# Performance work log

Hardware: AMD Instinct MI355X
Metric: run time of the kernel (lower is better)

## Reference

```python
import jax, jax.numpy as jnp
import numpy as np
from jax import lax

C = 512
B, H, W = 16, 32, 32
PROP_ROUNDS = 5


def _conv(x, w, b, pad):
    # x: [B,Cin,H,W], w: [Cout,Cin,kh,kw]
    y = lax.conv_general_dilated(x, w, (1, 1), [(pad, pad), (pad, pad)],
                                 dimension_numbers=('NCHW', 'OIHW', 'NCHW'))
    return y + b[None, :, None, None]


def _attention(ex, q):
    # torch: A = ex_flat^T @ q_flat ; Bm = softmax(A^T, dim=1) ; att = q_flat @ Bm
    b, c, h, w = q.shape
    ef = ex.reshape(b, c, h * w)   # [B,C,N] exemplar positions n
    qf = q.reshape(b, c, h * w)    # [B,C,M] query positions m
    A = jnp.einsum('bcn,bcm->bnm', ef, qf)   # [B,N,M]
    S = jax.nn.softmax(A, axis=-1)           # softmax over query positions m
    att = jnp.einsum('bcm,bnm->bcn', qf, S)  # [B,C,N]
    return att.reshape(b, c, h, w)


def _gru(x, h, w_r, b_r, w_u, b_u, w_c, b_c):
    # standard ConvGRUCell, kernel_size=1 (padding 0)
    xh = jnp.concatenate([x, h], axis=1)
    r = jax.nn.sigmoid(_conv(xh, w_r, b_r, 0))
    u = jax.nn.sigmoid(_conv(xh, w_u, b_u, 0))
    c = jnp.tanh(_conv(jnp.concatenate([x, r * h], axis=1), w_c, b_c, 0))
    return h * (1.0 - u) + c * u


def setup_inputs() -> dict:
    key = jax.random.key(0)
    ks = jax.random.split(key, 8)
    f = lambda k, s: jax.random.normal(k, s, dtype=jnp.float32)
    return {
        'input1': f(ks[0], (B, C, H, W)),
        'input2': f(ks[1], (B, C, H, W)),
        'input3': f(ks[2], (B, C, H, W)),
        'w_fusion': f(ks[3], (C, 2 * C, 3, 3)) * 0.01,
        'b_fusion': jnp.zeros((C,), jnp.float32),
        'w_out': f(ks[4], (C, 2 * C, 3, 3)) * 0.01,
        'b_out': jnp.zeros((C,), jnp.float32),
        'w_reset': f(ks[5], (C, 2 * C, 1, 1)) * 0.01,
        'b_reset': jnp.zeros((C,), jnp.float32),
        'w_update': f(ks[6], (C, 2 * C, 1, 1)) * 0.01,
        'b_update': jnp.zeros((C,), jnp.float32),
        'w_cand': f(ks[7], (C, 2 * C, 1, 1)) * 0.01,
        'b_cand': jnp.zeros((C,), jnp.float32),
    }


def reference(input1, input2, input3, w_fusion, b_fusion, w_out, b_out,
              w_reset, b_reset, w_update, b_update, w_cand, b_cand):
    # Batched over B (per-item torch loop is mathematically independent per item).
    ex, q, q1 = input1, input2, input3
    gru = lambda x, h: _gru(x, h, w_reset, b_reset, w_update, b_update, w_cand, b_cand)
    for _ in range(PROP_ROUNDS):
        a1 = _conv(jnp.concatenate([_attention(ex, q), _attention(ex, q1)], 1), w_fusion, b_fusion, 1)
        a2 = _conv(jnp.concatenate([_attention(q, ex), _attention(q, q1)], 1), w_fusion, b_fusion, 1)
        a3 = _conv(jnp.concatenate([_attention(q1, ex), _attention(q1, q)], 1), w_fusion, b_fusion, 1)
        ex, q, q1 = gru(a1, ex), gru(a2, q), gru(a3, q1)
    x1 = _conv(jnp.concatenate([ex, input1], 1), w_out, b_out, 1)
    x2 = _conv(jnp.concatenate([q, input2], 1), w_out, b_out, 1)
    x3 = _conv(jnp.concatenate([q1, input3], 1), w_out, b_out, 1)
    return (x1, x2, x3)
```

## Files before the change

kernel.cpp:

```cpp
#include <hip/hip_runtime.h>
#include <hip/hip_bf16.h>


using bf16 = __hip_bfloat16;
typedef __attribute__((ext_vector_type(8))) short bf16x8;
typedef __attribute__((ext_vector_type(4))) float floatx4;

#define MFMA_BF16(a, b, c) __builtin_amdgcn_mfma_f32_16x16x32_bf16((a), (b), (c), 0, 0, 0)

__device__ __forceinline__ void gload_lds16(const bf16* g, bf16* l) {
  __builtin_amdgcn_global_load_lds(
      (__attribute__((address_space(1))) void*)(g),
      (__attribute__((address_space(3))) void*)(l), 16, 0, 0);
}

__device__ __forceinline__ int swz_off(int row, int seg) {
  return row * 32 + ((seg ^ ((row >> 1) & 3)) << 3);
}

__device__ __forceinline__ void stage128x32_async(const bf16* src, int ld,
                                                  bf16* lds, int tid) {
  int r = tid >> 2;
  int seg_log = (((tid & 3) ^ ((tid >> 3) & 3))) * 8;
  gload_lds16(src + (size_t)r * ld + seg_log, lds + tid * 8);
  gload_lds16(src + (size_t)(r + 64) * ld + seg_log, lds + tid * 8 + 2048);
}

__device__ __forceinline__ void mfma_tile(const bf16* la, const bf16* lb,
                                          int wm, int wn, int fm, int fq,
                                          floatx4 (&acc)[4][4]) {
  bf16x8 af[4], bfr[4];
#pragma unroll
  for (int i = 0; i < 4; i++)
    af[i] = *(const bf16x8*)(la + swz_off(wm + i * 16 + fm, fq));
#pragma unroll
  for (int j = 0; j < 4; j++)
    bfr[j] = *(const bf16x8*)(lb + swz_off(wn + j * 16 + fm, fq));
#pragma unroll
  for (int i = 0; i < 4; i++)
#pragma unroll
    for (int j = 0; j < 4; j++)
      acc[i][j] = MFMA_BF16(af[i], bfr[j], acc[i][j]);
}

__device__ __forceinline__ float sigmoidf_(float x) { return 1.0f / (1.0f + __expf(-x)); }
__device__ __forceinline__ unsigned short bfbits(float x) {
  bf16 h = __float2bfloat16(x);
  return *reinterpret_cast<unsigned short*>(&h);
}

__global__ void k_detect(const unsigned short* __restrict__ in, int* __restrict__ flag) {
  if (threadIdx.x == 0 && blockIdx.x == 0) {
    int cnt = 0;
    for (int i = 0; i < 512; i++) {
      int e = (in[i] >> 7) & 0xFF;
      if (e >= 114 && e <= 140) cnt++;
      }
    *flag = (cnt >= 450) ? 1 : 0;
  }
}

__global__ __launch_bounds__(256) void k_cvt(const void* __restrict__ src,
                                             bf16* __restrict__ dst,
                                             const int* __restrict__ flag, int n) {
  int i = blockIdx.x * 256 + threadIdx.x;
  if (i >= n) return;
  if (*flag)
    dst[i] = ((const bf16*)src)[i];
  else
    dst[i] = __float2bfloat16(((const float*)src)[i]);
}

__global__ __launch_bounds__(256, 2) void k_gram(const bf16* __restrict__ X,
                                                 const bf16* __restrict__ Y,
                                                 float* __restrict__ G) {
  int b = blockIdx.z;
  const bf16* Ab = X + (size_t)b * 524288 + (size_t)blockIdx.x * 128 * 512;
  const bf16* Bb = Y + (size_t)b * 524288 + (size_t)blockIdx.y * 128 * 512;
  __shared__ __align__(16) bf16 la[4096], lb[4096];
  int tid = threadIdx.x, wave = tid >> 6, lane = tid & 63;
  int wm = (wave & 1) * 64, wn = (wave >> 1) * 64, fm = lane & 15, fq = lane >> 4;
  floatx4 acc[4][4] = {};
  for (int kc = 0; kc < 512; kc += 32) {
    __syncthreads();
    stage128x32_async(Ab + kc, 512, la, tid);
    stage128x32_async(Bb + kc, 512, lb, tid);
    __syncthreads();
    mfma_tile(la, lb, wm, wn, fm, fq, acc);
  }
  size_t gb = (size_t)b * 1048576;
  int row0 = blockIdx.x * 128 + wm + fq * 4;
  int col0 = blockIdx.y * 128 + wn + fm;
#pragma unroll
  for (int i = 0; i < 4; i++)
#pragma unroll
    for (int j = 0; j < 4; j++)
#pragma unroll
      for (int r = 0; r < 4; r++)
        G[gb + (size_t)(row0 + i * 16 + r) * 1024 + col0 + j * 16] = acc[i][j][r];
}

__global__ __launch_bounds__(256) void k_softmax(float* __restrict__ G) {
  size_t row = blockIdx.x;
  float* g = G + row * 1024;
  int tid = threadIdx.x, wave = tid >> 6, lane = tid & 63;
  float4 x = ((const float4*)g)[tid];
  float m = fmaxf(fmaxf(x.x, x.y), fmaxf(x.z, x.w));
  for (int off = 32; off > 0; off >>= 1) m = fmaxf(m, __shfl_xor(m, off));
  __shared__ float red[4], red2[4];
  if (lane == 0) red[wave] = m;
  __syncthreads();
  m = fmaxf(fmaxf(red[0], red[1]), fmaxf(red[2], red[3]));
  float e0 = __expf(x.x - m), e1 = __expf(x.y - m);
  float e2 = __expf(x.z - m), e3 = __expf(x.w - m);
  float s = e0 + e1 + e2 + e3;
  for (int off = 32; off > 0; off >>= 1) s += __shfl_xor(s, off);
  if (lane == 0) red2[wave] = s;
  __syncthreads();
  float inv = 1.0f / (red2[0] + red2[1] + red2[2] + red2[3]);
  ushort4 o;
  o.x = bfbits(e0 * inv); o.y = bfbits(e1 * inv);
  o.z = bfbits(e2 * inv); o.w = bfbits(e3 * inv);
  ((ushort4*)((bf16*)g))[tid] = o;
}

__global__ __launch_bounds__(256, 2) void k_att(const bf16* __restrict__ S,
                                                const bf16* __restrict__ Ycn,
                                                bf16* __restrict__ out) {
  int b = blockIdx.z;
  const bf16* Ab = S + (size_t)b * 2097152 + (size_t)blockIdx.x * 128 * 2048;
  const bf16* Bb = Ycn + (size_t)b * 524288 + (size_t)blockIdx.y * 128 * 1024;
  __shared__ __align__(16) bf16 la[4096], lb[4096];
  int tid = threadIdx.x, wave = tid >> 6, lane = tid & 63;
  int wm = (wave & 1) * 64, wn = (wave >> 1) * 64, fm = lane & 15, fq = lane >> 4;
  floatx4 acc[4][4] = {};
  for (int kc = 0; kc < 1024; kc += 32) {
    __syncthreads();
    stage128x32_async(Ab + kc, 2048, la, tid);
    stage128x32_async(Bb + kc, 1024, lb, tid);
    __syncthreads();
    mfma_tile(la, lb, wm, wn, fm, fq, acc);
  }
  size_t ob = (size_t)b * 524288;
  int row0 = blockIdx.x * 128 + wm + fq * 4;
  int col0 = blockIdx.y * 128 + wn + fm;
#pragma unroll
  for (int i = 0; i < 4; i++)
#pragma unroll
    for (int j = 0; j < 4; j++)
#pragma unroll
      for (int r = 0; r < 4; r++)
        out[ob + (size_t)(row0 + i * 16 + r) * 512 + col0 + j * 16] =
            __float2bfloat16(acc[i][j][r]);
}

__global__ __launch_bounds__(256, 2) void k_gru01(const bf16* __restrict__ xb,
                                                  const bf16* __restrict__ hb,
                                                  const bf16* __restrict__ wR,
                                                  const bf16* __restrict__ bR,
                                                  const bf16* __restrict__ wU,
                                                  const bf16* __restrict__ bU,
                                                  bf16* __restrict__ rh_out,
                                                  bf16* __restrict__ u_out) {
  size_t row0 = (size_t)blockIdx.x * 128;
  int y = blockIdx.y;
  bool isR = (y < 4);
  int yy = isR ? y : (y - 4);
  const bf16* W = (isR ? wR : wU) + (size_t)yy * 128 * 1024;
  const bf16* bias = isR ? bR : bU;
  bf16* outp = isR ? rh_out : u_out;
  __shared__ __align__(16) bf16 la[4096], lb[4096];
  int tid = threadIdx.x, wave = tid >> 6, lane = tid & 63;
  int wm = (wave & 1) * 64, wn = (wave >> 1) * 64, fm = lane & 15, fq = lane >> 4;
  floatx4 acc[4][4] = {};
  for (int kc = 0; kc < 1024; kc += 32) {
    __syncthreads();
    const bf16* s_ = (kc < 512) ? (xb + row0 * 512 + kc) : (hb + row0 * 512 + (kc - 512));
    stage128x32_async(s_, 512, la, tid);
    stage128x32_async(W + kc, 1024, lb, tid);
    __syncthreads();
    mfma_tile(la, lb, wm, wn, fm, fq, acc);
  }
  int r0 = wm + fq * 4;
  int c0 = yy * 128 + wn + fm;
#pragma unroll
  for (int i = 0; i < 4; i++)
#pragma unroll
    for (int j = 0; j < 4; j++) {
      int co = c0 + j * 16;
      float bj = __bfloat162float(bias[co]);
#pragma unroll
      for (int r = 0; r < 4; r++) {
        size_t idx = (row0 + r0 + i * 16 + r) * 512 + co;
        float v = sigmoidf_(acc[i][j][r] + bj);
        if (isR)
          outp[idx] = __float2bfloat16(v * __bfloat162float(hb[idx]));
        else
          outp[idx] = __float2bfloat16(v);
      }
    }
}

__global__ __launch_bounds__(256, 2) void k_gru2(const bf16* __restrict__ xb,
                                                 const bf16* __restrict__ rhb,
                                                 const bf16* __restrict__ W,
                                                 const bf16* __restrict__ bias,
                                                 bf16* __restrict__ h_state,
                                                 const bf16* __restrict__ u_buf) {
  size_t row0 = (size_t)blockIdx.x * 128;
  const bf16* Wb = W + (size_t)blockIdx.y * 128 * 1024;
  __shared__ __align__(16) bf16 la[4096], lb[4096];
  int tid = threadIdx.x, wave = tid >> 6, lane = tid & 63;
  int wm = (wave & 1) * 64, wn = (wave >> 1) * 64, fm = lane & 15, fq = lane >> 4;
  floatx4 acc[4][4] = {};
  for (int kc = 0; kc < 1024; kc += 32) {
    __syncthreads();
    const bf16* s_ = (kc < 512) ? (xb + row0 * 512 + kc) : (rhb + row0 * 512 + (kc - 512));
    stage128x32_async(s_, 512, la, tid);
    stage128x32_async(Wb + kc, 1024, lb, tid);
    __syncthreads();
    mfma_tile(la, lb, wm, wn, fm, fq, acc);
  }
  int r0 = wm + fq * 4;
  int c0 = blockIdx.y * 128 + wn + fm;
#pragma unroll
  for (int i = 0; i < 4; i++)
#pragma unroll
    for (int j = 0; j < 4; j++) {
      int co = c0 + j * 16;
      float bj = __bfloat162float(bias[co]);
#pragma unroll
      for (int r = 0; r < 4; r++) {
        size_t idx = (row0 + r0 + i * 16 + r) * 512 + co;
        float cv = tanhf(acc[i][j][r] + bj);
        float uu = __bfloat162float(u_buf[idx]);
        float h = __bfloat162float(h_state[idx]);
        h_state[idx] = __float2bfloat16(h * (1.0f - uu) + cv * uu);
      }
    }
}

__global__ __launch_bounds__(256, 2) void k_conv3(const bf16* __restrict__ src0,
                                                  const bf16* __restrict__ src1,
                                                  const bf16* __restrict__ wT,
                                                  const bf16* __restrict__ bias,
                                                  bf16* __restrict__ out) {
  int z = blockIdx.z;
  int y0 = blockIdx.x * 4;
  int co0 = blockIdx.y * 128;
  __shared__ __align__(16) bf16 lin[6528];
  __shared__ __align__(16) bf16 lw[2][4096];
  int tid = threadIdx.x, wave = tid >> 6, lane = tid & 63;
  int wm = (wave & 1) * 64, wn = (wave >> 1) * 64, fm = lane & 15, fq = lane >> 4;
  floatx4 acc[4][4] = {};
  const bf16* s0 = src0 + (size_t)z * 524288;
  const bf16* s1 = src1 + (size_t)z * 524288;
  int r_ = tid >> 2;
  int segl_ = (((tid & 3) ^ ((tid >> 3) & 3))) * 8;

  for (int cc = 0; cc < 32; cc++) {
    const bf16* sbase = (cc < 16) ? (s0 + cc * 32) : (s1 + (cc - 16) * 32);
    __syncthreads();
    {
      const bf16* wsrc = wT + (size_t)co0 * 1024 + cc * 32;
      gload_lds16(wsrc + (size_t)r_ * 1024 + segl_, lw[0] + tid * 8);
      gload_lds16(wsrc + (size_t)(r_ + 64) * 1024 + segl_, lw[0] + tid * 8 + 2048);
    }
#pragma unroll
    for (int k = 0; k < 4; k++) {
      int slot = k * 256 + tid;
      if (slot < 816) {
        int p = slot >> 2, sg = slot & 3;
        int yy = p / 34, xx = p - yy * 34;
        int y = y0 + yy - 1, x = xx - 1;
        bf16x8 v = {0, 0, 0, 0, 0, 0, 0, 0};
        if (y >= 0 && y <= 31 && x >= 0 && x <= 31)
          v = *(const bf16x8*)(sbase + (size_t)(y * 32 + x) * 512 + sg * 8);
        *(bf16x8*)(lin + swz_off(p, sg)) = v;
      }
    }
    __syncthreads();
#pragma unroll
    for (int t = 0; t < 9; t++) {
      if (t < 8) {
        const bf16* wsrc = wT + ((size_t)(t + 1) * 512 + co0) * 1024 + cc * 32;
        bf16* dstw = lw[(t + 1) & 1];
        gload_lds16(wsrc + (size_t)r_ * 1024 + segl_, dstw + tid * 8);
        gload_lds16(wsrc + (size_t)(r_ + 64) * 1024 + segl_, dstw + tid * 8 + 2048);
      }
      int dy = t / 3 - 1, dx = t % 3 - 1;
      bf16x8 af[4], bfr[4];
#pragma unroll
      for (int i = 0; i < 4; i++) {
        int j = wm + i * 16 + fm;
        int jy = j >> 5, jx = j & 31;
        int p = (jy + dy + 1) * 34 + (jx + dx + 1);
        af[i] = *(const bf16x8*)(lin + swz_off(p, fq));
      }
#pragma unroll
      for (int jj = 0; jj < 4; jj++)
        bfr[jj] = *(const bf16x8*)(lw[t & 1] + swz_off(wn + jj * 16 + fm, fq));
#pragma unroll
      for (int i = 0; i < 4; i++)
#pragma unroll
        for (int jj = 0; jj < 4; jj++)
          acc[i][jj] = MFMA_BF16(af[i], bfr[jj], acc[i][jj]);
      if (t < 8) __syncthreads();
    }
  }
  size_t ob = (size_t)z * 524288;
  int row0 = blockIdx.x * 128 + wm + fq * 4;
  int c0 = co0 + wn + fm;
#pragma unroll
  for (int i = 0; i < 4; i++)
#pragma unroll
    for (int jj = 0; jj < 4; jj++) {
      int co = c0 + jj * 16;
      float bj = __bfloat162float(bias[co]);
#pragma unroll
      for (int r = 0; r < 4; r++)
        out[ob + (size_t)(row0 + i * 16 + r) * 512 + co] =
            __float2bfloat16(acc[i][jj][r] + bj);
    }
}

__global__ __launch_bounds__(256) void k_transpose(const bf16* __restrict__ src,
                                                   bf16* __restrict__ dst,
                                                   int R, int C) {
  __shared__ bf16 t[32][33];
  size_t zoff = (size_t)blockIdx.z * R * C;
  int c0 = blockIdx.x * 32, r0 = blockIdx.y * 32;
  int x = threadIdx.x & 31, y4 = (threadIdx.x >> 5) * 4;
#pragma unroll
  for (int i = 0; i < 4; i++)
    t[y4 + i][x] = src[zoff + (size_t)(r0 + y4 + i) * C + c0 + x];
  __syncthreads();
#pragma unroll
  for (int i = 0; i < 4; i++)
    dst[zoff + (size_t)(c0 + y4 + i) * R + r0 + x] = t[x][y4 + i];
}

__global__ __launch_bounds__(256) void k_store(const bf16* __restrict__ src,
                                               void* __restrict__ dst,
                                               const int* __restrict__ flag) {
  __shared__ bf16 t[32][33];
  size_t zoff = (size_t)blockIdx.z * 524288;
  int c0 = blockIdx.x * 32, r0 = blockIdx.y * 32;
  int x = threadIdx.x & 31, y4 = (threadIdx.x >> 5) * 4;
#pragma unroll
  for (int i = 0; i < 4; i++)
    t[y4 + i][x] = src[zoff + (size_t)(r0 + y4 + i) * 512 + c0 + x];
  __syncthreads();
  bool isbf = (*flag != 0);
#pragma unroll
  for (int i = 0; i < 4; i++) {
    bf16 v = t[x][y4 + i];
    size_t o = zoff + (size_t)(c0 + y4 + i) * 1024 + r0 + x;
    if (isbf) ((bf16*)dst)[o] = v;
    else ((float*)dst)[o] = __bfloat162float(v);
  }
}

__global__ __launch_bounds__(256) void k_init(const void* __restrict__ in1,
                                              const void* __restrict__ in2,
                                              const void* __restrict__ in3,
                                              bf16* __restrict__ state_h,
                                              bf16* __restrict__ state_c,
                                              const int* __restrict__ flag) {
  int z = blockIdx.z, s = z >> 4, b = z & 15;
  const void* srcv = (s == 0 ? in1 : (s == 1 ? in2 : in3));
  bool isbf = (*flag != 0);
  size_t base = (size_t)b * 524288;
  size_t dz = (size_t)z * 524288;
  int n0 = blockIdx.x * 32, c0 = blockIdx.y * 32;
  __shared__ bf16 t[32][33];
  int x = threadIdx.x & 31, y4 = (threadIdx.x >> 5) * 4;
#pragma unroll
  for (int i = 0; i < 4; i++) {
    size_t off = base + (size_t)(c0 + y4 + i) * 1024 + n0 + x;
    bf16 v = isbf ? ((const bf16*)srcv)[off]
                  : __float2bfloat16(((const float*)srcv)[off]);
    t[y4 + i][x] = v;
    state_c[dz + (size_t)(c0 + y4 + i) * 1024 + n0 + x] = v;
  }
  __syncthreads();
#pragma unroll
  for (int i = 0; i < 4; i++)
    state_h[dz + (size_t)(n0 + y4 + i) * 512 + c0 + x] = t[x][y4 + i];
}

__global__ __launch_bounds__(256) void k_in_nhwc(const void* __restrict__ in1,
                                                 const void* __restrict__ in2,
                                                 const void* __restrict__ in3,
                                                 bf16* __restrict__ dst,
                                                 const int* __restrict__ flag) {
  int z = blockIdx.z, s = z >> 4, b = z & 15;
  const void* srcv = (s == 0 ? in1 : (s == 1 ? in2 : in3));
  bool isbf = (*flag != 0);
  size_t base = (size_t)b * 524288;
  size_t dz = (size_t)z * 524288;
  int n0 = blockIdx.x * 32, c0 = blockIdx.y * 32;
  __shared__ bf16 t[32][33];
  int x = threadIdx.x & 31, y4 = (threadIdx.x >> 5) * 4;
#pragma unroll
  for (int i = 0; i < 4; i++) {
    size_t off = base + (size_t)(c0 + y4 + i) * 1024 + n0 + x;
    t[y4 + i][x] = isbf ? ((const bf16*)srcv)[off]
                        : __float2bfloat16(((const float*)srcv)[off]);
  }
  __syncthreads();
#pragma unroll
  for (int i = 0; i < 4; i++)
    dst[dz + (size_t)(n0 + y4 + i) * 512 + c0 + x] = t[x][y4 + i];
}

__global__ __launch_bounds__(256) void k_wtrans(const void* __restrict__ w,
                                                bf16* __restrict__ wT,
                                                const int* __restrict__ flag) {
  int idx = blockIdx.x * 256 + threadIdx.x;
  bool isbf = (*flag != 0);
#pragma unroll
  for (int t = 0; t < 9; t++) {
    bf16 v = isbf ? ((const bf16*)w)[(size_t)idx * 9 + t]
                  : __float2bfloat16(((const float*)w)[(size_t)idx * 9 + t]);
    wT[(size_t)t * 524288 + idx] = v;
  }
}

extern "C" void kernel_launch(void* const* d_in, const int* in_sizes, int n_in,
                              void* d_out, int out_size, void* d_ws, size_t ws_size,
                              hipStream_t stream) {
  (void)in_sizes; (void)n_in; (void)out_size; (void)ws_size;
  const void* in1 = d_in[0];
  const void* in2 = d_in[1];
  const void* in3 = d_in[2];

  char* ws = (char*)d_ws;
  bf16* state_h = (bf16*)(ws + 0);
  bf16* state_c = (bf16*)(ws + 50331648);
  bf16* AttA    = (bf16*)(ws + 100663296);
  bf16* RHbuf   = (bf16*)(ws + 100663296);
  bf16* in_nhwc = (bf16*)(ws + 100663296);
  bf16* AttB    = (bf16*)(ws + 150994944);
  bf16* Ubuf    = (bf16*)(ws + 150994944);
  bf16* OutTmp  = (bf16*)(ws + 150994944);
  float* Gbuf   = (float*)(ws + 201326592);
  bf16* Sbuf    = (bf16*)(ws + 201326592);
  bf16* wT_out  = (bf16*)(ws + 201326592);
  bf16* wT_fus  = (bf16*)(ws + 234881024);
  bf16* wR      = (bf16*)(ws + 244318208);
  bf16* wU      = (bf16*)(ws + 245366784);
  bf16* wC      = (bf16*)(ws + 246415360);
  bf16* bF      = (bf16*)(ws + 247463936);
  bf16* bO      = (bf16*)(ws + 247465984);
  bf16* bR      = (bf16*)(ws + 247468032);
  bf16* bU      = (bf16*)(ws + 247470080);
  bf16* bC      = (bf16*)(ws + 247472128);
  int*  flag    = (int*)(ws + 247474176);
  bf16* Abuf    = (bf16*)d_out;

  const size_t SLICE = 16 * 1024 * 512;
  const size_t CHUNK = 8 * 1024 * 512;

  k_detect<<<1, 64, 0, stream>>>((const unsigned short*)d_in[0], flag);
  k_cvt<<<2048, 256, 0, stream>>>(d_in[7], wR, flag, 524288);
  k_cvt<<<2048, 256, 0, stream>>>(d_in[9], wU, flag, 524288);
  k_cvt<<<2048, 256, 0, stream>>>(d_in[11], wC, flag, 524288);
  k_cvt<<<2, 256, 0, stream>>>(d_in[4], bF, flag, 512);
  k_cvt<<<2, 256, 0, stream>>>(d_in[6], bO, flag, 512);
  k_cvt<<<2, 256, 0, stream>>>(d_in[8], bR, flag, 512);
  k_cvt<<<2, 256, 0, stream>>>(d_in[10], bU, flag, 512);
  k_cvt<<<2, 256, 0, stream>>>(d_in[12], bC, flag, 512);
  k_wtrans<<<2048, 256, 0, stream>>>(d_in[3], wT_fus, flag);
  k_init<<<dim3(32, 16, 48), 256, 0, stream>>>(in1, in2, in3, state_h, state_c, flag);

  const int sx[6] = {0, 0, 1, 1, 2, 2};
  const int sy[6] = {1, 2, 0, 2, 0, 1};
  for (int round = 0; round < 5; ++round) {
    for (int p = 0; p < 3; ++p) {
      for (int h = 0; h < 2; ++h) {
        int i = p * 2 + h;
        bf16* attdst = (h == 0 ? AttA : AttB) + p * SLICE;
        for (int cb = 0; cb < 2; ++cb) {
          size_t co = (size_t)cb * CHUNK;
          k_gram<<<dim3(8, 8, 8), 256, 0, stream>>>(
              state_h + sx[i] * SLICE + co, state_h + sy[i] * SLICE + co, Gbuf);
          k_softmax<<<8192, 256, 0, stream>>>(Gbuf);
          k_att<<<dim3(8, 4, 8), 256, 0, stream>>>(
              Sbuf, state_c + sy[i] * SLICE + co, attdst + co);
        }
      }
    }
    k_conv3<<<dim3(8, 4, 48), 256, 0, stream>>>(AttA, AttB, wT_fus, bF, Abuf);
    k_gru01<<<dim3(384, 8), 256, 0, stream>>>(Abuf, state_h, wR, bR, wU, bU,
                                              RHbuf, Ubuf);
    k_gru2<<<dim3(384, 4), 256, 0, stream>>>(Abuf, RHbuf, wC, bC, state_h, Ubuf);
    k_transpose<<<dim3(16, 32, 48), 256, 0, stream>>>(state_h, state_c, 1024, 512);
  }
  k_wtrans<<<2048, 256, 0, stream>>>(d_in[5], wT_out, flag);
  k_in_nhwc<<<dim3(32, 16, 48), 256, 0, stream>>>(in1, in2, in3, in_nhwc, flag);
  k_conv3<<<dim3(8, 4, 48), 256, 0, stream>>>(state_h, in_nhwc, wT_out, bO, OutTmp);
  k_store<<<dim3(16, 32, 48), 256, 0, stream>>>(OutTmp, d_out, flag);
}
```

Baseline: 7.290 ms.

## Software-pipeline conv3 with triple-buffered weights and register-prefetched input tile

Restructures the 3x3 conv main loop into a deeper pipeline. Weight slices are triple-buffered in LDS and issued two taps ahead across channel-chunk boundaries. The next input halo tile is prefetched into registers during the first tap and written to LDS at the end of the chunk. The __syncthreads calls are replaced with manual vmcnt/lgkmcnt waits, raw barriers, sched_barriers and setprio around the MFMAs, which aims to hide global-load latency. The cost is more LDS and more registers under a raised launch-bounds occupancy hint, and hand-counted waitcnts that are fragile to get right.

```diff
diff --git a/kernel.cpp b/kernel.cpp
--- a/kernel.cpp
+++ b/kernel.cpp
@@ -240,7 +240,7 @@
     }
 }
 
-__global__ __launch_bounds__(256, 2) void k_conv3(const bf16* __restrict__ src0,
+__global__ __launch_bounds__(256, 3) void k_conv3(const bf16* __restrict__ src0,
                                                   const bf16* __restrict__ src1,
                                                   const bf16* __restrict__ wT,
                                                   const bf16* __restrict__ bias,
@@ -249,7 +249,7 @@
   int y0 = blockIdx.x * 4;
   int co0 = blockIdx.y * 128;
   __shared__ __align__(16) bf16 lin[6528];
-  __shared__ __align__(16) bf16 lw[2][4096];
+  __shared__ __align__(16) bf16 lw[3][4096];
   int tid = threadIdx.x, wave = tid >> 6, lane = tid & 63;
   int wm = (wave & 1) * 64, wn = (wave >> 1) * 64, fm = lane & 15, fq = lane >> 4;
   floatx4 acc[4][4] = {};
@@ -258,36 +258,59 @@
   int r_ = tid >> 2;
   int segl_ = (((tid & 3) ^ ((tid >> 3) & 3))) * 8;
 
+  int sl_p[4], sl_sg[4], sl_off[4];
+  bool sl_v[4];
+#pragma unroll
+  for (int k = 0; k < 4; k++) {
+    int slot = k * 256 + tid;
+    int sl = slot < 816 ? slot : 815;
+    int p = sl >> 2, sg = sl & 3;
+    int yy = p / 34, xx = p - yy * 34;
+    int y = y0 + yy - 1, x = xx - 1;
+    sl_v[k] = (slot < 816) && (y >= 0) && (y <= 31) && (x >= 0) && (x <= 31);
+    int yc = min(max(y, 0), 31), xc = min(max(x, 0), 31);
+    sl_p[k] = p; sl_sg[k] = sg;
+    sl_off[k] = (yc * 32 + xc) * 512 + sg * 8;
+  }
+  bf16x8 lreg[4];
+  const bf16x8 zero8 = {0, 0, 0, 0, 0, 0, 0, 0};
+
+  auto lin_load = [&](int cc) {
+    const bf16* sb = (cc < 16) ? (s0 + cc * 32) : (s1 + (cc - 16) * 32);
+#pragma unroll
+    for (int k = 0; k < 4; k++)
+      lreg[k] = *(const bf16x8*)(sb + sl_off[k]);
+  };
+  auto lin_write = [&]() {
+#pragma unroll
+    for (int k = 0; k < 4; k++)
+      if (k * 256 + tid < 816)
+        *(bf16x8*)(lin + swz_off(sl_p[k], sl_sg[k])) = sl_v[k] ? lreg[k] : zero8;
+  };
+  auto issueW = [&](int cc, int t) {
+    const bf16* wsrc = wT + ((size_t)t * 512 + co0) * 1024 + cc * 32;
+    bf16* dst = lw[t % 3];
+    gload_lds16(wsrc + (size_t)r_ * 1024 + segl_, dst + tid * 8);
+    gload_lds16(wsrc + (size_t)(r_ + 64) * 1024 + segl_, dst + tid * 8 + 2048);
+  };
+
+  lin_load(0);
+  lin_write();
+  issueW(0, 0);
+  issueW(0, 1);
+  asm volatile("s_waitcnt lgkmcnt(0)" ::: "memory");
+
   for (int cc = 0; cc < 32; cc++) {
-    const bf16* sbase = (cc < 16) ? (s0 + cc * 32) : (s1 + (cc - 16) * 32);
-    __syncthreads();
-    {
-      const bf16* wsrc = wT + (size_t)co0 * 1024 + cc * 32;
-      gload_lds16(wsrc + (size_t)r_ * 1024 + segl_, lw[0] + tid * 8);
-      gload_lds16(wsrc + (size_t)(r_ + 64) * 1024 + segl_, lw[0] + tid * 8 + 2048);
-    }
-#pragma unroll
-    for (int k = 0; k < 4; k++) {
-      int slot = k * 256 + tid;
-      if (slot < 816) {
-        int p = slot >> 2, sg = slot & 3;
-        int yy = p / 34, xx = p - yy * 34;
-        int y = y0 + yy - 1, x = xx - 1;
-        bf16x8 v = {0, 0, 0, 0, 0, 0, 0, 0};
-        if (y >= 0 && y <= 31 && x >= 0 && x <= 31)
-          v = *(const bf16x8*)(sbase + (size_t)(y * 32 + x) * 512 + sg * 8);
-        *(bf16x8*)(lin + swz_off(p, sg)) = v;
-      }
-    }
-    __syncthreads();
 #pragma unroll
     for (int t = 0; t < 9; t++) {
-      if (t < 8) {
-        const bf16* wsrc = wT + ((size_t)(t + 1) * 512 + co0) * 1024 + cc * 32;
-        bf16* dstw = lw[(t + 1) & 1];
-        gload_lds16(wsrc + (size_t)r_ * 1024 + segl_, dstw + tid * 8);
-        gload_lds16(wsrc + (size_t)(r_ + 64) * 1024 + segl_, dstw + tid * 8 + 2048);
-      }
+      if (t == 1 || t == 2)
+        asm volatile("s_waitcnt vmcnt(6)" ::: "memory");
+      else
+        asm volatile("s_waitcnt vmcnt(2)" ::: "memory");
+      if (t == 0)
+        asm volatile("s_waitcnt lgkmcnt(0)" ::: "memory");
+      __builtin_amdgcn_s_barrier();
+      __builtin_amdgcn_sched_barrier(0);
       int dy = t / 3 - 1, dx = t % 3 - 1;
       bf16x8 af[4], bfr[4];
 #pragma unroll
@@ -299,15 +322,36 @@
       }
 #pragma unroll
       for (int jj = 0; jj < 4; jj++)
-        bfr[jj] = *(const bf16x8*)(lw[t & 1] + swz_off(wn + jj * 16 + fm, fq));
+        bfr[jj] = *(const bf16x8*)(lw[t % 3] + swz_off(wn + jj * 16 + fm, fq));
+      {
+        int tt = t + 2;
+        int ccn = cc + (tt >= 9 ? 1 : 0);
+        int tn = tt >= 9 ? tt - 9 : tt;
+        if (ccn >= 32) ccn = 0;
+        issueW(ccn, tn);
+      }
+      if (t == 0) {
+        __builtin_amdgcn_sched_barrier(0);
+        lin_load(cc < 31 ? cc + 1 : cc);
+        __builtin_amdgcn_sched_barrier(0);
+      }
+      asm volatile("s_waitcnt lgkmcnt(0)" ::: "memory");
+      __builtin_amdgcn_sched_barrier(0);
+      __builtin_amdgcn_s_setprio(1);
 #pragma unroll
       for (int i = 0; i < 4; i++)
 #pragma unroll
         for (int jj = 0; jj < 4; jj++)
           acc[i][jj] = MFMA_BF16(af[i], bfr[jj], acc[i][jj]);
-      if (t < 8) __syncthreads();
+      __builtin_amdgcn_s_setprio(0);
+      __builtin_amdgcn_sched_barrier(0);
     }
-  }
+    __builtin_amdgcn_s_barrier();
+    __builtin_amdgcn_sched_barrier(0);
+    lin_write();
+  }
+  asm volatile("s_waitcnt vmcnt(0)" ::: "memory");
+
   size_t ob = (size_t)z * 524288;
   int row0 = blockIdx.x * 128 + wm + fq * 4;
   int c0 = co0 + wn + fm;
```

New measurement: 7.024 ms. -3.7%, faster.
